# Optimization experiments

Hardware: AMD Instinct MI355X
Metric: run time of the kernel (lower is better)

Reference implementation:

```python
import jax, jax.numpy as jnp
import numpy as np

B, T, D, MP = 32, 256, 512, 20


def setup_inputs() -> dict:
    key = jax.random.key(0)
    k1, k2, k3 = jax.random.split(key, 3)
    reps_lt = jax.random.normal(k1, (B, T, D), dtype=jnp.float32)
    reps_rt = jax.random.normal(k2, (B, T, D), dtype=jnp.float32)
    kernel = jax.random.normal(k3, (1, 1, 1, MP, D), dtype=jnp.float32)
    return {"reps_lt": reps_lt, "reps_rt": reps_rt, "kernel": kernel}


def reference(reps_lt, reps_rt, kernel):
    # kernel: (1,1,1,m,d) -> (m,d)
    km = kernel.reshape(kernel.shape[-2], kernel.shape[-1])
    # scores[b,t,s,m] = sum_d lt[b,t,d] * km[m,d] * rt[b,s,d]
    # matches original broadcast-multiply + sum over d (cosine_norm=False path)
    scores = jnp.einsum('btd,md,bsd->btsm', reps_lt, km, reps_rt)
    match = jnp.tanh(scores)               # [b, t1, t2, m]
    return jnp.max(match, axis=2)          # max-pool over t2 -> [b, t1, m]
```

## Files before the change

### kernel.cpp

```cpp
#include <hip/hip_runtime.h>


constexpr int TT = 256;
constexpr int DD = 512;
constexpr int NM = 20;
constexpr int NB = 32;
constexpr int BM = 64;
constexpr int NK = 4;

typedef float f32x4 __attribute__((ext_vector_type(4)));
typedef int   i32x8 __attribute__((ext_vector_type(8)));

__device__ __forceinline__ unsigned pack_bf16(float lo, float hi) {
    unsigned ulo = __builtin_bit_cast(unsigned, lo);
    unsigned uhi = __builtin_bit_cast(unsigned, hi);
    return (ulo >> 16) | (uhi & 0xFFFF0000u);
}

__device__ __forceinline__ unsigned pk4_fp8(float a, float b, float c, float d) {
    unsigned r = __builtin_amdgcn_cvt_pk_fp8_f32(a, b, 0, false);
    return __builtin_amdgcn_cvt_pk_fp8_f32(c, d, r, true);
}

__device__ __forceinline__ float blo(unsigned u) { return __builtin_bit_cast(float, u << 16); }
__device__ __forceinline__ float bhi(unsigned u) { return __builtin_bit_cast(float, u); }

__device__ __forceinline__ i32x8 mk8(uint4 a, uint4 b) {
    i32x8 v;
    v[0] = (int)a.x; v[1] = (int)a.y; v[2] = (int)a.z; v[3] = (int)a.w;
    v[4] = (int)b.x; v[5] = (int)b.y; v[6] = (int)b.z; v[7] = (int)b.w;
    return v;
}

__global__ __launch_bounds__(256)
void cast_inputs(const float* __restrict__ lt, const float* __restrict__ rt,
                 unsigned short* __restrict__ ltb, unsigned char* __restrict__ rtf)
{
    const int half = (int)gridDim.x >> 1;
    if ((int)blockIdx.x < half) {
        size_t base = ((size_t)blockIdx.x * 256 + threadIdx.x) * 8;
        float4 a = *(const float4*)(lt + base);
        float4 b = *(const float4*)(lt + base + 4);
        uint4 w;
        w.x = pack_bf16(a.x, a.y);
        w.y = pack_bf16(a.z, a.w);
        w.z = pack_bf16(b.x, b.y);
        w.w = pack_bf16(b.z, b.w);
        *(uint4*)(ltb + base) = w;
    } else {
        size_t base = ((size_t)(blockIdx.x - half) * 256 + threadIdx.x) * 8;
        float4 a = *(const float4*)(rt + base);
        float4 b = *(const float4*)(rt + base + 4);
        uint2 o;
        o.x = pk4_fp8(a.x, a.y, a.z, a.w);
        o.y = pk4_fp8(b.x, b.y, b.z, b.w);
        *(uint2*)(rtf + base) = o;
    }
}

__global__ __launch_bounds__(256, 2)
void mp_match_mx(const unsigned short* __restrict__ ltb, const unsigned char* __restrict__ rtf,
                 const float* __restrict__ km, float* __restrict__ out)
{
    __shared__ __attribute__((aligned(16))) uint4 Ash[BM * 33];
    __shared__ __attribute__((aligned(16))) float maxbuf[4][BM];

    const int f  = blockIdx.x;
    const int c8 = f & 7;
    const int i  = f >> 3;
    const int b  = c8 + 8 * (i / 80);
    const int j  = i % 80;
    const int m  = j >> 2;
    const int t0 = (j & 3) * BM;

    const int tid  = threadIdx.x;
    const int w    = tid >> 6;
    const int lane = tid & 63;
    const int l15  = lane & 15;
    const int l4   = lane >> 4;
    const int ws   = w * 64;

    const unsigned short* ltB = ltb + ((size_t)b * TT + t0) * DD;
    const unsigned char*  rtB = rtf + (size_t)b * TT * DD;
    const float*          kmp = km  + (size_t)m * DD;

    auto loadB = [&](int kk, uint4* d) {
#pragma unroll
        for (int jj = 0; jj < 4; ++jj) {
            const unsigned char* p = rtB + (size_t)(ws + jj * 16 + l15) * DD + kk * 128 + l4 * 32;
            d[jj * 2]     = *(const uint4*)p;
            d[jj * 2 + 1] = *(const uint4*)(p + 16);
        }
    };

    uint4 b0[8], b1[8];
    loadB(0, b0);

    const int cc = tid & 31, r0 = (tid >> 5) * 8;
    const float4 kA = *(const float4*)(kmp + cc * 16);
    const float4 kB = *(const float4*)(kmp + cc * 16 + 4);
    const float4 kC = *(const float4*)(kmp + cc * 16 + 8);
    const float4 kD = *(const float4*)(kmp + cc * 16 + 12);
#pragma unroll
    for (int r = 0; r < 8; ++r) {
        const unsigned short* src = ltB + (size_t)(r0 + r) * DD + cc * 16;
        uint4 h0 = *(const uint4*)src;
        uint4 h1 = *(const uint4*)(src + 8);
        uint4 o;
        o.x = pk4_fp8(blo(h0.x) * kA.x, bhi(h0.x) * kA.y, blo(h0.y) * kA.z, bhi(h0.y) * kA.w);
        o.y = pk4_fp8(blo(h0.z) * kB.x, bhi(h0.z) * kB.y, blo(h0.w) * kB.z, bhi(h0.w) * kB.w);
        o.z = pk4_fp8(blo(h1.x) * kC.x, bhi(h1.x) * kC.y, blo(h1.y) * kC.z, bhi(h1.y) * kC.w);
        o.w = pk4_fp8(blo(h1.z) * kD.x, bhi(h1.z) * kD.y, blo(h1.w) * kD.z, bhi(h1.w) * kD.w);
        Ash[(r0 + r) * 33 + cc] = o;
    }
    __syncthreads();

    auto loadA = [&](int kk, uint4* d) {
#pragma unroll
        for (int ii = 0; ii < 4; ++ii) {
            int base = (ii * 16 + l15) * 33 + kk * 8 + l4 * 2;
            d[ii * 2]     = Ash[base];
            d[ii * 2 + 1] = Ash[base + 1];
        }
    };

    f32x4 acc[4][4] = {};
    uint4 aA[8], aB[8];
    loadA(0, aA);

#pragma unroll
    for (int kk = 0; kk < NK; ++kk) {
        uint4* bc = (kk & 1) ? b1 : b0;
        uint4* bn = (kk & 1) ? b0 : b1;
        const uint4* ac = (kk & 1) ? aB : aA;
        uint4* an = (kk & 1) ? aA : aB;
        if (kk + 1 < NK) {
            loadB(kk + 1, bn);
            loadA(kk + 1, an);
        }
        i32x8 av[4], bv[4];
#pragma unroll
        for (int ii = 0; ii < 4; ++ii) av[ii] = mk8(ac[ii * 2], ac[ii * 2 + 1]);
#pragma unroll
        for (int jj = 0; jj < 4; ++jj) bv[jj] = mk8(bc[jj * 2], bc[jj * 2 + 1]);
#pragma unroll
        for (int ii = 0; ii < 4; ++ii)
#pragma unroll
            for (int jj = 0; jj < 4; ++jj)
                acc[ii][jj] = __builtin_amdgcn_mfma_scale_f32_16x16x128_f8f6f4(
                    av[ii], bv[jj], acc[ii][jj], 0, 0, 0, 127, 0, 127);
    }

#pragma unroll
    for (int ii = 0; ii < 4; ++ii) {
        f32x4 v = acc[ii][0];
#pragma unroll
        for (int jj = 1; jj < 4; ++jj) {
            v.x = fmaxf(v.x, acc[ii][jj].x);
            v.y = fmaxf(v.y, acc[ii][jj].y);
            v.z = fmaxf(v.z, acc[ii][jj].z);
            v.w = fmaxf(v.w, acc[ii][jj].w);
        }
#pragma unroll
        for (int off = 1; off < 16; off <<= 1) {
            v.x = fmaxf(v.x, __shfl_xor(v.x, off, 64));
            v.y = fmaxf(v.y, __shfl_xor(v.y, off, 64));
            v.z = fmaxf(v.z, __shfl_xor(v.z, off, 64));
            v.w = fmaxf(v.w, __shfl_xor(v.w, off, 64));
        }
        if (l15 == 0)
            *(f32x4*)&maxbuf[w][ii * 16 + l4 * 4] = v;
    }
    __syncthreads();
    if (tid < BM) {
        float v = fmaxf(fmaxf(maxbuf[0][tid], maxbuf[1][tid]),
                        fmaxf(maxbuf[2][tid], maxbuf[3][tid]));
        out[((size_t)b * TT + t0 + tid) * NM + m] = tanhf(v);
    }
}

typedef short bf16x8 __attribute__((ext_vector_type(8)));

__global__ __launch_bounds__(256, 2)
void mp_match_kernel(const float* __restrict__ lt, const float* __restrict__ rt,
                     const float* __restrict__ km, float* __restrict__ out)
{
    __shared__ __attribute__((aligned(16))) unsigned short Ash[2][4][128][8];
    __shared__ __attribute__((aligned(16))) unsigned short Bsh2[2][4][256][8];
    __shared__ __attribute__((aligned(16))) float maxbuf[2][128];

    const int ttile = blockIdx.x, m = blockIdx.y, b = blockIdx.z;
    const int t0 = ttile * 128;
    const int tid = threadIdx.x, wave = tid >> 6, lane = tid & 63;
    const int l15 = lane & 15, l4 = lane >> 4;
    const int wt = (wave & 1) * 64, wsi = wave >> 1;

    const float* ltp = lt + ((size_t)b * TT + t0) * DD;
    const float* rtp = rt + (size_t)b * TT * DD;
    const float* kmp = km + (size_t)m * DD;
    const int a_t = tid >> 1, a_h = tid & 1;

    f32x4 acc[4][8] = {};

    auto stage = [&](int kk, int buf) {
        const int d0 = kk * 32;
        const float* ap = ltp + (size_t)a_t * DD + d0 + a_h * 16;
        const float* kp = kmp + d0 + a_h * 16;
#pragma unroll
        for (int q = 0; q < 2; ++q) {
            float4 x0 = *(const float4*)(ap + q * 8);
            float4 x1 = *(const float4*)(ap + q * 8 + 4);
            float4 k0 = *(const float4*)(kp + q * 8);
            float4 k1 = *(const float4*)(kp + q * 8 + 4);
            uint4 wv;
            wv.x = pack_bf16(x0.x * k0.x, x0.y * k0.y);
            wv.y = pack_bf16(x0.z * k0.z, x0.w * k0.w);
            wv.z = pack_bf16(x1.x * k1.x, x1.y * k1.y);
            wv.w = pack_bf16(x1.z * k1.z, x1.w * k1.w);
            *(uint4*)&Ash[buf][a_h * 2 + q][a_t][0] = wv;
        }
        const float* bp = rtp + (size_t)tid * DD + d0;
#pragma unroll
        for (int p = 0; p < 4; ++p) {
            float4 y0 = *(const float4*)(bp + p * 8);
            float4 y1 = *(const float4*)(bp + p * 8 + 4);
            uint4 wv;
            wv.x = pack_bf16(y0.x, y0.y);
            wv.y = pack_bf16(y0.z, y0.w);
            wv.z = pack_bf16(y1.x, y1.y);
            wv.w = pack_bf16(y1.z, y1.w);
            *(uint4*)&Bsh2[buf][p][tid][0] = wv;
        }
    };

    stage(0, 0);
    for (int kk = 0; kk < 16; ++kk) {
        const int buf = kk & 1;
        __syncthreads();
        bf16x8 af[4], bfv[8];
#pragma unroll
        for (int i2 = 0; i2 < 4; ++i2)
            af[i2] = *(const bf16x8*)&Ash[buf][l4][wt + i2 * 16 + l15][0];
#pragma unroll
        for (int j2 = 0; j2 < 8; ++j2)
            bfv[j2] = *(const bf16x8*)&Bsh2[buf][l4][wsi * 128 + j2 * 16 + l15][0];
        if (kk + 1 < 16) stage(kk + 1, buf ^ 1);
#pragma unroll
        for (int i2 = 0; i2 < 4; ++i2)
#pragma unroll
            for (int j2 = 0; j2 < 8; ++j2)
                acc[i2][j2] = __builtin_amdgcn_mfma_f32_16x16x32_bf16(af[i2], bfv[j2], acc[i2][j2], 0, 0, 0);
    }
#pragma unroll
    for (int i2 = 0; i2 < 4; ++i2) {
        f32x4 v = acc[i2][0];
#pragma unroll
        for (int j2 = 1; j2 < 8; ++j2) {
            v.x = fmaxf(v.x, acc[i2][j2].x); v.y = fmaxf(v.y, acc[i2][j2].y);
            v.z = fmaxf(v.z, acc[i2][j2].z); v.w = fmaxf(v.w, acc[i2][j2].w);
        }
#pragma unroll
        for (int off = 1; off < 16; off <<= 1) {
            v.x = fmaxf(v.x, __shfl_xor(v.x, off, 64));
            v.y = fmaxf(v.y, __shfl_xor(v.y, off, 64));
            v.z = fmaxf(v.z, __shfl_xor(v.z, off, 64));
            v.w = fmaxf(v.w, __shfl_xor(v.w, off, 64));
        }
        if (l15 == 0) *(f32x4*)&maxbuf[wsi][wt + i2 * 16 + l4 * 4] = v;
    }
    __syncthreads();
    if (tid < 128) {
        float v = fmaxf(maxbuf[0][tid], maxbuf[1][tid]);
        out[((size_t)b * TT + t0 + tid) * NM + m] = tanhf(v);
    }
}

extern "C" void kernel_launch(void* const* d_in, const int* in_sizes, int n_in,
                              void* d_out, int out_size, void* d_ws, size_t ws_size,
                              hipStream_t stream) {
    const float* lt  = (const float*)d_in[0];
    const float* rt  = (const float*)d_in[1];
    const float* km  = (const float*)d_in[2];
    float*       out = (float*)d_out;

    const size_t elems = (size_t)NB * TT * DD;
    const size_t ltbB  = elems * sizeof(unsigned short);
    const size_t rtfB  = elems;

    if (ws_size >= ltbB + rtfB) {
        unsigned short* ltb = (unsigned short*)d_ws;
        unsigned char*  rtf = (unsigned char*)((char*)d_ws + ltbB);
        cast_inputs<<<4096, 256, 0, stream>>>(lt, rt, ltb, rtf);
        mp_match_mx<<<2560, 256, 0, stream>>>(ltb, rtf, km, out);
    } else {
        mp_match_kernel<<<dim3(2, NM, NB), 256, 0, stream>>>(lt, rt, km, out);
    }
}
```

Measured before the change: 123.8 us.

## Pre-swizzle FP8 rt into MFMA fragment order and stream via global_load_lds

```diff
diff --git a/kernel.cpp b/kernel.cpp
--- a/kernel.cpp
+++ b/kernel.cpp
@@ -6,7 +6,6 @@
 constexpr int NM = 20;
 constexpr int NB = 32;
 constexpr int BM = 64;
-constexpr int NK = 4;
 
 typedef float f32x4 __attribute__((ext_vector_type(4)));
 typedef int   i32x8 __attribute__((ext_vector_type(8)));
@@ -32,13 +31,19 @@
     return v;
 }
 
+__device__ __forceinline__ void gld_lds16(const void* g, void* l) {
+    __builtin_amdgcn_global_load_lds(
+        (const __attribute__((address_space(1))) void*)g,
+        (__attribute__((address_space(3))) void*)l, 16, 0, 0);
+}
+
 __global__ __launch_bounds__(256)
 void cast_inputs(const float* __restrict__ lt, const float* __restrict__ rt,
                  unsigned short* __restrict__ ltb, unsigned char* __restrict__ rtf)
 {
-    const int half = (int)gridDim.x >> 1;
-    if ((int)blockIdx.x < half) {
-        size_t base = ((size_t)blockIdx.x * 256 + threadIdx.x) * 8;
+    const int bid = (int)blockIdx.x;
+    if (bid < 2048) {
+        size_t base = ((size_t)bid * 256 + threadIdx.x) * 8;
         float4 a = *(const float4*)(lt + base);
         float4 b = *(const float4*)(lt + base + 4);
         uint4 w;
@@ -48,21 +53,34 @@
         w.w = pack_bf16(b.z, b.w);
         *(uint4*)(ltb + base) = w;
     } else {
-        size_t base = ((size_t)(blockIdx.x - half) * 256 + threadIdx.x) * 8;
-        float4 a = *(const float4*)(rt + base);
-        float4 b = *(const float4*)(rt + base + 4);
-        uint2 o;
-        o.x = pk4_fp8(a.x, a.y, a.z, a.w);
-        o.y = pk4_fp8(b.x, b.y, b.z, b.w);
-        *(uint2*)(rtf + base) = o;
-    }
-}
-
-__global__ __launch_bounds__(256, 2)
+        const unsigned o = (unsigned)(bid - 2048) * 256 + threadIdx.x;
+        const int lane = o & 63;
+        const int h    = (o >> 6) & 1;
+        const int g    = (o >> 7) & 15;
+        const int kk   = (o >> 11) & 3;
+        const int b    = o >> 13;
+        const int s    = g * 16 + (lane & 15);
+        const int d0   = kk * 128 + (lane >> 4) * 32 + h * 16;
+        const float* p = rt + ((size_t)b * TT + s) * DD + d0;
+        float4 x0 = *(const float4*)p;
+        float4 x1 = *(const float4*)(p + 4);
+        float4 x2 = *(const float4*)(p + 8);
+        float4 x3 = *(const float4*)(p + 12);
+        uint4 w;
+        w.x = pk4_fp8(x0.x, x0.y, x0.z, x0.w);
+        w.y = pk4_fp8(x1.x, x1.y, x1.z, x1.w);
+        w.z = pk4_fp8(x2.x, x2.y, x2.z, x2.w);
+        w.w = pk4_fp8(x3.x, x3.y, x3.z, x3.w);
+        *(uint4*)(rtf + (size_t)o * 16) = w;
+    }
+}
+
+__global__ __launch_bounds__(256, 3)
 void mp_match_mx(const unsigned short* __restrict__ ltb, const unsigned char* __restrict__ rtf,
                  const float* __restrict__ km, float* __restrict__ out)
 {
     __shared__ __attribute__((aligned(16))) uint4 Ash[BM * 33];
+    __shared__ __attribute__((aligned(16))) unsigned char Bsh[2][8192];
     __shared__ __attribute__((aligned(16))) float maxbuf[4][BM];
 
     const int f  = blockIdx.x;
@@ -78,23 +96,20 @@
     const int lane = tid & 63;
     const int l15  = lane & 15;
     const int l4   = lane >> 4;
-    const int ws   = w * 64;
 
     const unsigned short* ltB = ltb + ((size_t)b * TT + t0) * DD;
-    const unsigned char*  rtB = rtf + (size_t)b * TT * DD;
+    const unsigned char*  rtT = rtf + (size_t)b * (TT * DD);
     const float*          kmp = km  + (size_t)m * DD;
 
-    auto loadB = [&](int kk, uint4* d) {
-#pragma unroll
-        for (int jj = 0; jj < 4; ++jj) {
-            const unsigned char* p = rtB + (size_t)(ws + jj * 16 + l15) * DD + kk * 128 + l4 * 32;
-            d[jj * 2]     = *(const uint4*)p;
-            d[jj * 2 + 1] = *(const uint4*)(p + 16);
-        }
+    auto stageB = [&](int u) {
+        const int kk = u >> 2, q = u & 3;
+        const unsigned char* g = rtT + kk * 32768 + (q * 4 + w) * 2048 + lane * 16;
+        unsigned char* l = &Bsh[u & 1][w * 2048];
+        gld_lds16(g, l);
+        gld_lds16(g + 1024, l + 1024);
     };
 
-    uint4 b0[8], b1[8];
-    loadB(0, b0);
+    stageB(0);
 
     const int cc = tid & 31, r0 = (tid >> 5) * 8;
     const float4 kA = *(const float4*)(kmp + cc * 16);
@@ -115,51 +130,42 @@
     }
     __syncthreads();
 
-    auto loadA = [&](int kk, uint4* d) {
-#pragma unroll
-        for (int ii = 0; ii < 4; ++ii) {
-            int base = (ii * 16 + l15) * 33 + kk * 8 + l4 * 2;
-            d[ii * 2]     = Ash[base];
-            d[ii * 2 + 1] = Ash[base + 1];
-        }
-    };
-
     f32x4 acc[4][4] = {};
-    uint4 aA[8], aB[8];
-    loadA(0, aA);
-
-#pragma unroll
-    for (int kk = 0; kk < NK; ++kk) {
-        uint4* bc = (kk & 1) ? b1 : b0;
-        uint4* bn = (kk & 1) ? b0 : b1;
-        const uint4* ac = (kk & 1) ? aB : aA;
-        uint4* an = (kk & 1) ? aA : aB;
-        if (kk + 1 < NK) {
-            loadB(kk + 1, bn);
-            loadA(kk + 1, an);
-        }
-        i32x8 av[4], bv[4];
-#pragma unroll
-        for (int ii = 0; ii < 4; ++ii) av[ii] = mk8(ac[ii * 2], ac[ii * 2 + 1]);
-#pragma unroll
-        for (int jj = 0; jj < 4; ++jj) bv[jj] = mk8(bc[jj * 2], bc[jj * 2 + 1]);
+    i32x8 av[4];
+
+#pragma unroll
+    for (int u = 0; u < 16; ++u) {
+        const int kk = u >> 2, q = u & 3;
+        if (u + 1 < 16) {
+            stageB(u + 1);
+            asm volatile("s_waitcnt vmcnt(2)" ::: "memory");
+        } else {
+            asm volatile("s_waitcnt vmcnt(0)" ::: "memory");
+        }
+        if (q == 0) {
+#pragma unroll
+            for (int ii = 0; ii < 4; ++ii) {
+                const int base = (ii * 16 + l15) * 33 + kk * 8 + l4 * 2;
+                av[ii] = mk8(Ash[base], Ash[base + 1]);
+            }
+        }
+        const uint4* bp = (const uint4*)&Bsh[u & 1][w * 2048];
+        i32x8 bv = mk8(bp[lane], bp[64 + lane]);
 #pragma unroll
         for (int ii = 0; ii < 4; ++ii)
-#pragma unroll
-            for (int jj = 0; jj < 4; ++jj)
-                acc[ii][jj] = __builtin_amdgcn_mfma_scale_f32_16x16x128_f8f6f4(
-                    av[ii], bv[jj], acc[ii][jj], 0, 0, 0, 127, 0, 127);
+            acc[ii][q] = __builtin_amdgcn_mfma_scale_f32_16x16x128_f8f6f4(
+                av[ii], bv, acc[ii][q], 0, 0, 0, 127, 0, 127);
     }
 
 #pragma unroll
     for (int ii = 0; ii < 4; ++ii) {
         f32x4 v = acc[ii][0];
 #pragma unroll
-        for (int jj = 1; jj < 4; ++jj) {
-            v.x = fmaxf(v.x, acc[ii][jj].x);
-            v.y = fmaxf(v.y, acc[ii][jj].y);
-            v.z = fmaxf(v.z, acc[ii][jj].z);
-            v.w = fmaxf(v.w, acc[ii][jj].w);
+        for (int q = 1; q < 4; ++q) {
+            v.x = fmaxf(v.x, acc[ii][q].x);
+            v.y = fmaxf(v.y, acc[ii][q].y);
+            v.z = fmaxf(v.z, acc[ii][q].z);
+            v.w = fmaxf(v.w, acc[ii][q].w);
         }
 #pragma unroll
         for (int off = 1; off < 16; off <<= 1) {
@@ -290,7 +296,7 @@
     if (ws_size >= ltbB + rtfB) {
         unsigned short* ltb = (unsigned short*)d_ws;
         unsigned char*  rtf = (unsigned char*)((char*)d_ws + ltbB);
-        cast_inputs<<<4096, 256, 0, stream>>>(lt, rt, ltb, rtf);
+        cast_inputs<<<3072, 256, 0, stream>>>(lt, rt, ltb, rtf);
         mp_match_mx<<<2560, 256, 0, stream>>>(ltb, rtf, km, out);
     } else {
         mp_match_kernel<<<dim3(2, NM, NB), 256, 0, stream>>>(lt, rt, km, out);
```

Measured after the change: 116.5 us. 1.06x faster.
